# Kernel optimization log

Measured on AMD Instinct MI355X. Metric: run time of the kernel, lower is better.

The kernel has to match this reference:

```python
import jax, jax.numpy as jnp
import numpy as np

BITS = 8

def _hilbert_distance(grid, bits=BITS):
    # Skilling's algorithm: 3D grid coords -> Hilbert curve distance. grid: [N,3] int64.
    X = grid.astype(np.int64).copy()
    n = X.shape[1]
    M = 1 << (bits - 1)
    Q = M
    while Q > 1:
        P = Q - 1
        for i in range(n):
            hi = (X[:, i] & Q) != 0
            X[:, 0] = np.where(hi, X[:, 0] ^ P, X[:, 0])
            t = np.where(hi, 0, (X[:, 0] ^ X[:, i]) & P)
            X[:, 0] ^= t
            X[:, i] ^= t
        Q >>= 1
    for i in range(1, n):
        X[:, i] ^= X[:, i - 1]
    t = np.zeros(X.shape[0], dtype=np.int64)
    Q = M
    while Q > 1:
        t = np.where((X[:, n - 1] & Q) != 0, t ^ (Q - 1), t)
        Q >>= 1
    X ^= t[:, None]
    h = np.zeros(X.shape[0], dtype=np.int64)
    for b in range(bits - 1, -1, -1):
        for i in range(n):
            h = (h << 1) | ((X[:, i] >> b) & 1)
    return h

def _orders(x_np, bits=BITS):
    B, N, _ = x_np.shape
    oh = np.zeros((B, N), dtype=np.int64)
    ot = np.zeros((B, N), dtype=np.int64)
    gmax = (1 << bits) - 1
    for b in range(B):
        pts = x_np[b]
        mins, maxs = pts.min(0), pts.max(0)
        span = np.maximum(maxs - mins, 1e-6)
        norm = (pts - mins) / span
        g = np.clip(norm * gmax, 0, gmax).astype(np.int64)
        oh[b] = np.argsort(_hilbert_distance(g, bits), kind='stable')
        gt = np.clip(norm[:, ::-1] * gmax, 0, gmax).astype(np.int64)
        ot[b] = np.argsort(_hilbert_distance(gt, bits), kind='stable')
    return oh, ot

def setup_inputs() -> dict:
    key = jax.random.key(0)
    ks = jax.random.split(key, 12)
    B, N, E = 4, 2048, 128
    NB, DS, DC, EXP, NC = 2, 16, 4, 2, 40
    DI = E * EXP
    DR = max(1, (E + 15) // 16)
    x = jax.random.normal(ks[0], (B, N, 3), jnp.float32)
    oh, ot = _orders(np.asarray(x))
    # dt_proj bias = softplus^-1(dt), dt ~ LogUniform(1e-3, 0.1)
    dt = jnp.exp(jax.random.uniform(ks[1], (NB, DI)) * (np.log(0.1) - np.log(0.001)) + np.log(0.001))
    dtproj_b = dt + jnp.log(-jnp.expm1(-dt))
    return dict(
        x=x,
        order_h=jnp.asarray(oh), order_t=jnp.asarray(ot),
        pe_w=jax.random.normal(ks[2], (E, 3)) * 0.3, pe_b=jnp.zeros((E,)),
        gamma=jnp.ones((2, E)), beta=jnp.zeros((2, E)),
        ln_g=jnp.ones((NB, E)), ln_b=jnp.zeros((NB, E)),
        inproj_w=jax.random.normal(ks[3], (NB, 2 * DI, E)) * (E ** -0.5),
        conv_w=jax.random.normal(ks[4], (NB, DI, DC)) * 0.3,
        conv_b=jnp.zeros((NB, DI)),
        xproj_w=jax.random.normal(ks[5], (NB, DR + 2 * DS, DI)) * (DI ** -0.5),
        dtproj_w=jax.random.normal(ks[6], (NB, DI, DR)) * (DR ** -0.5),
        dtproj_b=dtproj_b,
        A_log=jnp.tile(jnp.log(jnp.arange(1, DS + 1, dtype=jnp.float32))[None, None], (NB, DI, 1)),
        Dp=jnp.ones((NB, DI)),
        outproj_w=jax.random.normal(ks[7], (NB, E, DI)) * (DI ** -0.5),
        hn_g=jnp.ones((E,)), hn_b=jnp.zeros((E,)),
        fc_w=jax.random.normal(ks[8], (NC, E)) * (E ** -0.5),
        fc_b=jnp.zeros((NC,)),
    )

def _ln(x, g, b):
    m = jnp.mean(x, -1, keepdims=True)
    v = jnp.mean((x - m) ** 2, -1, keepdims=True)
    return (x - m) / jnp.sqrt(v + 1e-5) * g + b

def _block(h, g, bb, inw, cw, cb, xw, dtw, dtb, Alog, Dv, outw):
    B, L, E = h.shape
    DI, DC = cw.shape
    DR = dtw.shape[1]
    DS = Alog.shape[1]
    xn = _ln(h, g, bb)
    uz = xn @ inw.T                       # [B, L, 2*DI]
    u, z = uz[..., :DI], uz[..., DI:]
    # depthwise causal conv (kernel DC, left pad DC-1)
    up = jnp.pad(u, ((0, 0), (DC - 1, 0), (0, 0)))
    uc = cb + sum(up[:, k:k + L, :] * cw[:, k] for k in range(DC))
    uc = jax.nn.silu(uc)
    xdbl = uc @ xw.T                      # [B, L, DR+2*DS]
    dt = xdbl[..., :DR]
    Bv = xdbl[..., DR:DR + DS]
    Cv = xdbl[..., DR + DS:]
    delta = jax.nn.softplus(dt @ dtw.T + dtb)  # [B, L, DI]
    A = -jnp.exp(Alog)                    # [DI, DS]
    def step(hst, xs):
        d, ut, bt, ct = xs                # [B,DI],[B,DI],[B,DS],[B,DS]
        hst = jnp.exp(d[:, :, None] * A[None]) * hst + (d * ut)[:, :, None] * bt[:, None, :]
        y = jnp.einsum('bds,bs->bd', hst, ct) + Dv * ut
        return hst, y
    h0 = jnp.zeros((B, DI, DS), h.dtype)
    _, ys = jax.lax.scan(step, h0, (delta.transpose(1, 0, 2), uc.transpose(1, 0, 2),
                                    Bv.transpose(1, 0, 2), Cv.transpose(1, 0, 2)))
    y = ys.transpose(1, 0, 2) * jax.nn.silu(z)
    return h + y @ outw.T

def reference(x, order_h, order_t, pe_w, pe_b, gamma, beta, ln_g, ln_b,
              inproj_w, conv_w, conv_b, xproj_w, dtproj_w, dtproj_b,
              A_log, Dp, outproj_w, hn_g, hn_b, fc_w, fc_b):
    pts_h = jnp.take_along_axis(x, order_h[..., None], axis=1)
    pts_t = jnp.take_along_axis(x, order_t[..., None], axis=1)
    th = (pts_h @ pe_w.T + pe_b) * gamma[0] + beta[0]
    tt = (pts_t @ pe_w.T + pe_b) * gamma[1] + beta[1]
    h = jnp.concatenate([th, tt], axis=1)  # [B, 2N, E]
    for i in range(ln_g.shape[0]):
        h = _block(h, ln_g[i], ln_b[i], inproj_w[i], conv_w[i], conv_b[i], xproj_w[i],
                   dtproj_w[i], dtproj_b[i], A_log[i], Dp[i], outproj_w[i])
    h = _ln(h, hn_g, hn_b)
    return h.mean(axis=1) @ fc_w.T + fc_b
```

## Files before the change

### kernel.cpp

```cpp
#include <hip/hip_runtime.h>
#include <hip/hip_bf16.h>
#include <math.h>

#define BATCH 4
#define NPTS  2048
#define L     4096
#define E     128
#define DI    256
#define DS    16
#define DRR   8
#define DCV   4
#define NBLK  2
#define NC    40
#define XDW   40
#define ROWS  (BATCH*L)
#define CH    32
#define NCH   128

typedef unsigned short u16;
typedef short short8 __attribute__((ext_vector_type(8)));
typedef float f32x4v __attribute__((ext_vector_type(4)));

__device__ __forceinline__ u16 f2bf(float x) {
  unsigned u = __float_as_uint(x);
  u = u + 0x7FFFu + ((u >> 16) & 1u);
  return (u16)(u >> 16);
}
__device__ __forceinline__ float bf2f(u16 h) {
  return __uint_as_float(((unsigned)h) << 16);
}
__device__ __forceinline__ float softplusf(float x) {
  if (x > 20.f) return x;
  float t = __builtin_amdgcn_exp2f(x * 1.44269504f);
  return 0.69314718f * __builtin_amdgcn_logf(1.f + t);
}

__global__ void embed_ln_split(const float* __restrict__ x,
                               const int* __restrict__ oh, const int* __restrict__ ot,
                               const float* __restrict__ pe_w, const float* __restrict__ pe_b,
                               const float* __restrict__ gamma, const float* __restrict__ beta,
                               const float* __restrict__ g, const float* __restrict__ bb,
                               float* __restrict__ h, u16* __restrict__ dhi, u16* __restrict__ dlo) {
  int wave = threadIdx.x >> 6;
  int lane = threadIdx.x & 63;
  int row = blockIdx.x * 4 + wave;
  int n = row % L;
  int b = row / L;
  int gi = (n >= NPTS) ? 1 : 0;
  int nn = n - gi * NPTS;
  int src = gi ? ot[b * NPTS + nn] : oh[b * NPTS + nn];
  const float* xp = x + ((size_t)b * NPTS + src) * 3;
  float p0 = xp[0], p1 = xp[1], p2 = xp[2];
  int e0 = lane, e1 = lane + 64;
  float v0 = pe_b[e0] + p0 * pe_w[e0 * 3] + p1 * pe_w[e0 * 3 + 1] + p2 * pe_w[e0 * 3 + 2];
  float v1 = pe_b[e1] + p0 * pe_w[e1 * 3] + p1 * pe_w[e1 * 3 + 1] + p2 * pe_w[e1 * 3 + 2];
  v0 = v0 * gamma[gi * E + e0] + beta[gi * E + e0];
  v1 = v1 * gamma[gi * E + e1] + beta[gi * E + e1];
  size_t base = (size_t)row * E;
  h[base + e0] = v0;
  h[base + e1] = v1;
  float s1 = v0 + v1, s2 = v0 * v0 + v1 * v1;
  #pragma unroll
  for (int off = 32; off > 0; off >>= 1) {
    s1 += __shfl_xor(s1, off);
    s2 += __shfl_xor(s2, off);
  }
  float m = s1 * (1.0f / E);
  float var = s2 * (1.0f / E) - m * m;
  float inv = rsqrtf(var + 1e-5f);
  float o0 = (v0 - m) * inv * g[e0] + bb[e0];
  float o1 = (v1 - m) * inv * g[e1] + bb[e1];
  u16 h0 = f2bf(o0), h1 = f2bf(o1);
  dhi[base + e0] = h0; dhi[base + e1] = h1;
  dlo[base + e0] = f2bf(o0 - bf2f(h0));
  dlo[base + e1] = f2bf(o1 - bf2f(h1));
}

__global__ void split_all(const float* __restrict__ inproj, const float* __restrict__ outw,
                          const float* __restrict__ xw,
                          u16* __restrict__ wihi, u16* __restrict__ wilo,
                          u16* __restrict__ wohi, u16* __restrict__ wolo,
                          u16* __restrict__ wxhi, u16* __restrict__ wxlo) {
  const int n1 = NBLK * 2 * DI * E;
  const int n2 = NBLK * E * DI;
  const int n3 = NBLK * XDW * DI;
  int i = blockIdx.x * 256 + threadIdx.x;
  if (i < n1) {
    float v = inproj[i];
    u16 h = f2bf(v);
    wihi[i] = h; wilo[i] = f2bf(v - bf2f(h));
  } else if (i < n1 + n2) {
    int j = i - n1;
    float v = outw[j];
    u16 h = f2bf(v);
    wohi[j] = h; wolo[j] = f2bf(v - bf2f(h));
  } else if (i < n1 + n2 + n3) {
    int j = i - n1 - n2;
    float v = xw[j];
    u16 h = f2bf(v);
    wxhi[j] = h; wxlo[j] = f2bf(v - bf2f(h));
  }
}

template<int BN, int ACC>
__global__ __launch_bounds__(256)
void mfma_gemm_lds(const u16* __restrict__ Ahi, const u16* __restrict__ Alo,
                   const u16* __restrict__ Bhi, const u16* __restrict__ Blo,
                   float* __restrict__ C, int M, int N, int K, int ldc) {
  constexpr int BM = 128, BK = 64, PITCH = 72;
  constexpr int MSUB = (BN == 128) ? 4 : 2;
  constexpr int NSUB = 4;
  __shared__ u16 sA[2][BM][PITCH];
  __shared__ u16 sB[2][BN][PITCH];
  int tid = threadIdx.x;
  int wave = tid >> 6, lane = tid & 63, quad = lane >> 4, l16 = lane & 15;
  int rowBase = blockIdx.x * BM, colBase = blockIdx.y * BN;
  int wrow = (BN == 128) ? (wave >> 1) * 64 : wave * 32;
  int wcol = (BN == 128) ? (wave & 1) * 64 : 0;
  f32x4v acc[MSUB][NSUB] = {};
  for (int k0 = 0; k0 < K; k0 += BK) {
    #pragma unroll
    for (int hl = 0; hl < 2; hl++) {
      const u16* srcA = hl ? Alo : Ahi;
      #pragma unroll
      for (int c = 0; c < BM * 8 / 256; c++) {
        int ch = c * 256 + tid;
        int row = ch >> 3, kc = ch & 7;
        float4 v = *(const float4*)(srcA + (size_t)(rowBase + row) * K + k0 + kc * 8);
        *(float4*)&sA[hl][row][kc * 8] = v;
      }
      const u16* srcB = hl ? Blo : Bhi;
      #pragma unroll
      for (int c = 0; c < BN * 8 / 256; c++) {
        int ch = c * 256 + tid;
        int row = ch >> 3, kc = ch & 7;
        float4 v = *(const float4*)(srcB + (size_t)(colBase + row) * K + k0 + kc * 8);
        *(float4*)&sB[hl][row][kc * 8] = v;
      }
    }
    __syncthreads();
    short8 afh[MSUB][2], afl[MSUB][2];
    #pragma unroll
    for (int i = 0; i < MSUB; i++)
      #pragma unroll
      for (int kf = 0; kf < 2; kf++) {
        afh[i][kf] = *(const short8*)&sA[0][wrow + i * 16 + l16][kf * 32 + quad * 8];
        afl[i][kf] = *(const short8*)&sA[1][wrow + i * 16 + l16][kf * 32 + quad * 8];
      }
    #pragma unroll
    for (int j = 0; j < NSUB; j++)
      #pragma unroll
      for (int kf = 0; kf < 2; kf++) {
        short8 bh = *(const short8*)&sB[0][wcol + j * 16 + l16][kf * 32 + quad * 8];
        short8 bl = *(const short8*)&sB[1][wcol + j * 16 + l16][kf * 32 + quad * 8];
        #pragma unroll
        for (int i = 0; i < MSUB; i++) {
          acc[i][j] = __builtin_amdgcn_mfma_f32_16x16x32_bf16(afh[i][kf], bh, acc[i][j], 0, 0, 0);
          acc[i][j] = __builtin_amdgcn_mfma_f32_16x16x32_bf16(afh[i][kf], bl, acc[i][j], 0, 0, 0);
          acc[i][j] = __builtin_amdgcn_mfma_f32_16x16x32_bf16(afl[i][kf], bh, acc[i][j], 0, 0, 0);
        }
      }
    __syncthreads();
  }
  int orow0 = rowBase + wrow + quad * 4;
  #pragma unroll
  for (int i = 0; i < MSUB; i++) {
    #pragma unroll
    for (int j = 0; j < NSUB; j++) {
      int cc = colBase + wcol + j * 16 + l16;
      #pragma unroll
      for (int r = 0; r < 4; r++) {
        size_t idx = (size_t)(orow0 + i * 16 + r) * ldc + cc;
        if (ACC) C[idx] += acc[i][j][r];
        else     C[idx] = acc[i][j][r];
      }
    }
  }
}

__global__ __launch_bounds__(256)
void conv_xproj(const float* __restrict__ uz, const float* __restrict__ cw,
                const float* __restrict__ cb,
                const u16* __restrict__ xwhi, const u16* __restrict__ xwlo,
                float* __restrict__ xdbl) {
  constexpr int RB = 16, UPITCH = DI + 8;
  __shared__ u16 sUhi[RB][UPITCH];
  __shared__ u16 sUlo[RB][UPITCH];
  int d = threadIdx.x;
  int r0 = blockIdx.x * RB;
  int t0 = r0 % L;
  const size_t US = 2 * DI;
  float w0 = cw[d * DCV], w1 = cw[d * DCV + 1], w2 = cw[d * DCV + 2], w3 = cw[d * DCV + 3];
  float bias = cb[d];
  float uwin[RB + 3];
  #pragma unroll
  for (int j = 0; j < RB + 3; j++) {
    int t = t0 + j - 3;
    uwin[j] = (t >= 0) ? uz[(size_t)(r0 + j - 3) * US + d] : 0.f;
  }
  #pragma unroll
  for (int j = 0; j < RB; j++) {
    float a = bias + w0 * uwin[j] + w1 * uwin[j + 1] + w2 * uwin[j + 2] + w3 * uwin[j + 3];
    float v = a / (1.f + __expf(-a));
    u16 hh = f2bf(v);
    sUhi[j][d] = hh;
    sUlo[j][d] = f2bf(v - bf2f(hh));
  }
  __syncthreads();
  int wave = threadIdx.x >> 6, lane = threadIdx.x & 63;
  int quad = lane >> 4, l16 = lane & 15;
  if (wave < 3) {
    int col = wave * 16 + l16;
    int colc = (col < XDW) ? col : 0;
    const u16* bhp = xwhi + (size_t)colc * DI;
    const u16* blp = xwlo + (size_t)colc * DI;
    f32x4v acc = {};
    #pragma unroll
    for (int ks = 0; ks < DI / 32; ks++) {
      short8 ah = *(const short8*)&sUhi[l16][ks * 32 + quad * 8];
      short8 al = *(const short8*)&sUlo[l16][ks * 32 + quad * 8];
      short8 bh = *(const short8*)(bhp + ks * 32 + quad * 8);
      short8 bl = *(const short8*)(blp + ks * 32 + quad * 8);
      acc = __builtin_amdgcn_mfma_f32_16x16x32_bf16(ah, bh, acc, 0, 0, 0);
      acc = __builtin_amdgcn_mfma_f32_16x16x32_bf16(ah, bl, acc, 0, 0, 0);
      acc = __builtin_amdgcn_mfma_f32_16x16x32_bf16(al, bh, acc, 0, 0, 0);
      acc = __builtin_amdgcn_mfma_f32_16x16x32_bf16(al, bl, acc, 0, 0, 0);
    }
    if (col < XDW) {
      #pragma unroll
      for (int r = 0; r < 4; r++)
        xdbl[(size_t)(r0 + quad * 4 + r) * XDW + col] = acc[r];
    }
  }
}

__global__ __launch_bounds__(256, 4)
void scan_passA(const float* __restrict__ uz, const float* __restrict__ xdbl,
                const float* __restrict__ dtw, const float* __restrict__ dtb,
                const float* __restrict__ A_log,
                const float* __restrict__ cw, const float* __restrict__ cb,
                float* __restrict__ hloc, float* __restrict__ sumd) {
  int b = blockIdx.x / NCH, c = blockIdx.x % NCH;
  int d = threadIdx.x;
  __shared__ float Bsh[CH][DS];
  __shared__ float Dsh[CH][DRR];
  for (int i = threadIdx.x; i < CH * DS; i += 256) {
    int tt = i >> 4, s = i & 15;
    Bsh[tt][s] = xdbl[((size_t)b * L + c * CH + tt) * XDW + DRR + s];
  }
  {
    int i = threadIdx.x;
    int td = i >> 3, q = i & 7;
    Dsh[td][q] = xdbl[((size_t)b * L + c * CH + td) * XDW + q];
  }
  const size_t US = 2 * DI;
  const float* up = uz + ((size_t)b * L + c * CH) * US + d;
  float cw0 = cw[d * DCV], cw1 = cw[d * DCV + 1], cw2 = cw[d * DCV + 2], cw3 = cw[d * DCV + 3];
  float cbias = cb[d];
  float um0, um1, um2;
  if (c == 0) { um0 = um1 = um2 = 0.f; }
  else {
    um0 = up[-3 * (ptrdiff_t)US];
    um1 = up[-2 * (ptrdiff_t)US];
    um2 = up[-1 * (ptrdiff_t)US];
  }
  float ucur = up[0];
  float Av[DS];
  #pragma unroll
  for (int s = 0; s < DS; s++) Av[s] = -__expf(A_log[d * DS + s]);
  bool fastE = true;
  #pragma unroll
  for (int s = 0; s < DS; s++)
    fastE = fastE && (fabsf(Av[s] + (float)(s + 1)) <= 1e-3f * (s + 1));
  float4 wd0 = *(const float4*)(dtw + d * DRR);
  float4 wd1 = *(const float4*)(dtw + d * DRR + 4);
  float dbias = dtb[d];
  __syncthreads();
  float st[DS] = {};
  float sd = 0.f;
  #pragma unroll
  for (int t0 = 0; t0 < CH; t0++) {
    float unext = (t0 + 1 < CH) ? up[(size_t)(t0 + 1) * US] : 0.f;
    float a = cbias + cw0 * um0 + cw1 * um1 + cw2 * um2 + cw3 * ucur;
    float utv = a / (1.f + __expf(-a));
    um0 = um1; um1 = um2; um2 = ucur; ucur = unext;
    float4 D0 = *(const float4*)&Dsh[t0][0];
    float4 D1 = *(const float4*)&Dsh[t0][4];
    float v = dbias + D0.x * wd0.x + D0.y * wd0.y + D0.z * wd0.z + D0.w * wd0.w
                    + D1.x * wd1.x + D1.y * wd1.y + D1.z * wd1.z + D1.w * wd1.w;
    float dl = softplusf(v);
    sd += dl;
    float du = dl * utv;
    float4 B0 = *(const float4*)&Bsh[t0][0];
    float4 B1 = *(const float4*)&Bsh[t0][4];
    float4 B2 = *(const float4*)&Bsh[t0][8];
    float4 B3 = *(const float4*)&Bsh[t0][12];
    float Bv[DS] = {B0.x, B0.y, B0.z, B0.w, B1.x, B1.y, B1.z, B1.w,
                    B2.x, B2.y, B2.z, B2.w, B3.x, B3.y, B3.z, B3.w};
    if (fastE) {
      float e1 = __expf(-dl);
      float er = 1.f;
      #pragma unroll
      for (int s = 0; s < DS; s++) {
        er *= e1;
        st[s] = er * st[s] + du * Bv[s];
      }
    } else {
      #pragma unroll
      for (int s = 0; s < DS; s++) {
        float aa = __expf(dl * Av[s]);
        st[s] = aa * st[s] + du * Bv[s];
      }
    }
  }
  size_t base = (((size_t)b * NCH + c) * DI + d) * DS;
  *(float4*)&hloc[base + 0]  = float4{st[0], st[1], st[2], st[3]};
  *(float4*)&hloc[base + 4]  = float4{st[4], st[5], st[6], st[7]};
  *(float4*)&hloc[base + 8]  = float4{st[8], st[9], st[10], st[11]};
  *(float4*)&hloc[base + 12] = float4{st[12], st[13], st[14], st[15]};
  sumd[((size_t)b * NCH + c) * DI + d] = sd;
}

#define PB_G 16
__global__ __launch_bounds__(64)
void scan_passB(const float* __restrict__ A_log, const float* __restrict__ hloc,
                const float* __restrict__ sumd, float* __restrict__ hinit) {
  int tid = threadIdx.x;
  int dgroup = blockIdx.x % (DI / 4);
  int b = blockIdx.x / (DI / 4);
  int d = dgroup * 4 + (tid >> 4);
  int s = tid & 15;
  float Av = -__expf(A_log[d * DS + s]);
  size_t off = (size_t)b * NCH * DI * DS + dgroup * 64 + tid;
  size_t soff = (size_t)b * NCH * DI + d;
  const size_t HST = (size_t)DI * DS;
  float bv[PB_G], sd[PB_G], bvn[PB_G], sdn[PB_G];
  #pragma unroll
  for (int j = 0; j < PB_G; j++) {
    bv[j] = hloc[off + j * HST];
    sd[j] = sumd[soff + j * DI];
  }
  float X = 0.f;
  for (int g = 0; g < NCH / PB_G; g++) {
    if (g + 1 < NCH / PB_G) {
      #pragma unroll
      for (int j = 0; j < PB_G; j++) {
        bvn[j] = hloc[off + (j + PB_G) * HST];
        sdn[j] = sumd[soff + (j + PB_G) * DI];
      }
    }
    #pragma unroll
    for (int j = 0; j < PB_G; j++) {
      float a = __expf(Av * sd[j]);
      hinit[off + j * HST] = X;
      X = a * X + bv[j];
    }
    #pragma unroll
    for (int j = 0; j < PB_G; j++) { bv[j] = bvn[j]; sd[j] = sdn[j]; }
    off += PB_G * HST;
    soff += PB_G * DI;
  }
}

template<int VARIANT>
__global__ __launch_bounds__(256, 2)
void scan_passC_out(const float* __restrict__ uz, const float* __restrict__ xdbl,
                    const float* __restrict__ dtw, const float* __restrict__ dtb,
                    const float* __restrict__ A_log, const float* __restrict__ Dp,
                    const float* __restrict__ cw, const float* __restrict__ cb,
                    const float* __restrict__ hinit,
                    const u16* __restrict__ wohi, const u16* __restrict__ wolo,
                    float* __restrict__ h, const float* __restrict__ g,
                    const float* __restrict__ bb, u16* __restrict__ dhi,
                    u16* __restrict__ dlo, float* __restrict__ partial) {
  constexpr int YP = DI + 8;
  constexpr int HP = E + 4;
  int b = blockIdx.x / NCH, c = blockIdx.x % NCH;
  int d = threadIdx.x;
  __shared__ float Bsh[CH][DS];
  __shared__ float Csh[CH][DS];
  __shared__ float Dsh[CH][DRR];
  __shared__ u16 sYhi[CH][YP];
  __shared__ u16 sYlo[CH][YP];
  __shared__ float hsm[CH][HP];
  __shared__ float red[4][E];
  for (int i = threadIdx.x; i < CH * DS; i += 256) {
    int tt = i >> 4, s = i & 15;
    size_t rb = ((size_t)b * L + c * CH + tt) * XDW;
    Bsh[tt][s] = xdbl[rb + DRR + s];
    Csh[tt][s] = xdbl[rb + DRR + DS + s];
  }
  {
    int i = threadIdx.x;
    int td = i >> 3, q = i & 7;
    Dsh[td][q] = xdbl[((size_t)b * L + c * CH + td) * XDW + q];
  }
  const size_t US = 2 * DI;
  const float* up = uz + ((size_t)b * L + c * CH) * US + d;
  const float* zp = up + DI;
  float cw0 = cw[d * DCV], cw1 = cw[d * DCV + 1], cw2 = cw[d * DCV + 2], cw3 = cw[d * DCV + 3];
  float cbias = cb[d];
  float um0, um1, um2;
  if (c == 0) { um0 = um1 = um2 = 0.f; }
  else {
    um0 = up[-3 * (ptrdiff_t)US];
    um1 = up[-2 * (ptrdiff_t)US];
    um2 = up[-1 * (ptrdiff_t)US];
  }
  float ucur = up[0];
  float zcur = zp[0];
  float st[DS];
  size_t hbase = (((size_t)b * NCH + c) * DI + d) * DS;
  {
    float4 h0 = *(const float4*)&hinit[hbase + 0];
    float4 h1 = *(const float4*)&hinit[hbase + 4];
    float4 h2 = *(const float4*)&hinit[hbase + 8];
    float4 h3 = *(const float4*)&hinit[hbase + 12];
    st[0]=h0.x; st[1]=h0.y; st[2]=h0.z; st[3]=h0.w;
    st[4]=h1.x; st[5]=h1.y; st[6]=h1.z; st[7]=h1.w;
    st[8]=h2.x; st[9]=h2.y; st[10]=h2.z; st[11]=h2.w;
    st[12]=h3.x; st[13]=h3.y; st[14]=h3.z; st[15]=h3.w;
  }
  float Av[DS];
  #pragma unroll
  for (int s = 0; s < DS; s++) Av[s] = -__expf(A_log[d * DS + s]);
  bool fastE = true;
  #pragma unroll
  for (int s = 0; s < DS; s++)
    fastE = fastE && (fabsf(Av[s] + (float)(s + 1)) <= 1e-3f * (s + 1));
  float4 wd0 = *(const float4*)(dtw + d * DRR);
  float4 wd1 = *(const float4*)(dtw + d * DRR + 4);
  float dbias = dtb[d];
  float Dv = Dp[d];
  __syncthreads();
  #pragma unroll 8
  for (int t0 = 0; t0 < CH; t0++) {
    float unext = (t0 + 1 < CH) ? up[(size_t)(t0 + 1) * US] : 0.f;
    float znext = (t0 + 1 < CH) ? zp[(size_t)(t0 + 1) * US] : 0.f;
    float a = cbias + cw0 * um0 + cw1 * um1 + cw2 * um2 + cw3 * ucur;
    float utv = a / (1.f + __expf(-a));
    um0 = um1; um1 = um2; um2 = ucur; ucur = unext;
    float4 D0 = *(const float4*)&Dsh[t0][0];
    float4 D1 = *(const float4*)&Dsh[t0][4];
    float v = dbias + D0.x * wd0.x + D0.y * wd0.y + D0.z * wd0.z + D0.w * wd0.w
                    + D1.x * wd1.x + D1.y * wd1.y + D1.z * wd1.z + D1.w * wd1.w;
    float dl = softplusf(v);
    float du = dl * utv;
    float acc = Dv * utv;
    float4 B0 = *(const float4*)&Bsh[t0][0];
    float4 B1 = *(const float4*)&Bsh[t0][4];
    float4 B2 = *(const float4*)&Bsh[t0][8];
    float4 B3 = *(const float4*)&Bsh[t0][12];
    float4 C0 = *(const float4*)&Csh[t0][0];
    float4 C1 = *(const float4*)&Csh[t0][4];
    float4 C2 = *(const float4*)&Csh[t0][8];
    float4 C3 = *(const float4*)&Csh[t0][12];
    float Bv[DS] = {B0.x, B0.y, B0.z, B0.w, B1.x, B1.y, B1.z, B1.w,
                    B2.x, B2.y, B2.z, B2.w, B3.x, B3.y, B3.z, B3.w};
    float Cv[DS] = {C0.x, C0.y, C0.z, C0.w, C1.x, C1.y, C1.z, C1.w,
                    C2.x, C2.y, C2.z, C2.w, C3.x, C3.y, C3.z, C3.w};
    if (fastE) {
      float e1 = __expf(-dl);
      float er = 1.f;
      #pragma unroll
      for (int s = 0; s < DS; s++) {
        er *= e1;
        st[s] = er * st[s] + du * Bv[s];
        acc += st[s] * Cv[s];
      }
    } else {
      #pragma unroll
      for (int s = 0; s < DS; s++) {
        float aa = __expf(dl * Av[s]);
        st[s] = aa * st[s] + du * Bv[s];
        acc += st[s] * Cv[s];
      }
    }
    float zz = zcur; zcur = znext;
    float yv = acc * (zz / (1.f + __expf(-zz)));
    u16 hh = f2bf(yv);
    sYhi[t0][d] = hh;
    sYlo[t0][d] = f2bf(yv - bf2f(hh));
  }
  __syncthreads();
  int wave = d >> 6, lane = d & 63, quad = lane >> 4, l16 = lane & 15;
  f32x4v oacc[2][2] = {};
  #pragma unroll
  for (int ks = 0; ks < DI / 32; ks++) {
    short8 a0h = *(const short8*)&sYhi[l16][ks * 32 + quad * 8];
    short8 a0l = *(const short8*)&sYlo[l16][ks * 32 + quad * 8];
    short8 a1h = *(const short8*)&sYhi[16 + l16][ks * 32 + quad * 8];
    short8 a1l = *(const short8*)&sYlo[16 + l16][ks * 32 + quad * 8];
    #pragma unroll
    for (int j = 0; j < 2; j++) {
      int col = wave * 32 + j * 16 + l16;
      short8 bh = *(const short8*)(wohi + (size_t)col * DI + ks * 32 + quad * 8);
      short8 bl = *(const short8*)(wolo + (size_t)col * DI + ks * 32 + quad * 8);
      oacc[0][j] = __builtin_amdgcn_mfma_f32_16x16x32_bf16(a0h, bh, oacc[0][j], 0, 0, 0);
      oacc[0][j] = __builtin_amdgcn_mfma_f32_16x16x32_bf16(a0h, bl, oacc[0][j], 0, 0, 0);
      oacc[0][j] = __builtin_amdgcn_mfma_f32_16x16x32_bf16(a0l, bh, oacc[0][j], 0, 0, 0);
      oacc[1][j] = __builtin_amdgcn_mfma_f32_16x16x32_bf16(a1h, bh, oacc[1][j], 0, 0, 0);
      oacc[1][j] = __builtin_amdgcn_mfma_f32_16x16x32_bf16(a1h, bl, oacc[1][j], 0, 0, 0);
      oacc[1][j] = __builtin_amdgcn_mfma_f32_16x16x32_bf16(a1l, bh, oacc[1][j], 0, 0, 0);
    }
  }
  size_t rr0 = (size_t)b * L + c * CH;
  #pragma unroll
  for (int i = 0; i < 2; i++) {
    #pragma unroll
    for (int j = 0; j < 2; j++) {
      int col = wave * 32 + j * 16 + l16;
      #pragma unroll
      for (int r = 0; r < 4; r++) {
        int row = i * 16 + quad * 4 + r;
        float v = h[(rr0 + row) * E + col] + oacc[i][j][r];
        hsm[row][col] = v;
        if (VARIANT == 0) h[(rr0 + row) * E + col] = v;
      }
    }
  }
  __syncthreads();
  float g0 = g[lane], g1 = g[lane + 64], b0 = bb[lane], b1 = bb[lane + 64];
  float pa0 = 0.f, pa1 = 0.f;
  for (int jj = 0; jj < 8; jj++) {
    int row = wave * 8 + jj;
    float x0 = hsm[row][lane], x1 = hsm[row][lane + 64];
    float s1 = x0 + x1, s2 = x0 * x0 + x1 * x1;
    #pragma unroll
    for (int off = 32; off > 0; off >>= 1) {
      s1 += __shfl_xor(s1, off);
      s2 += __shfl_xor(s2, off);
    }
    float m = s1 * (1.0f / E);
    float var = s2 * (1.0f / E) - m * m;
    float inv = rsqrtf(var + 1e-5f);
    float o0 = (x0 - m) * inv * g0 + b0;
    float o1 = (x1 - m) * inv * g1 + b1;
    if (VARIANT == 0) {
      size_t base = (rr0 + row) * E;
      u16 h0 = f2bf(o0), h1 = f2bf(o1);
      dhi[base + lane]      = h0;
      dhi[base + lane + 64] = h1;
      dlo[base + lane]      = f2bf(o0 - bf2f(h0));
      dlo[base + lane + 64] = f2bf(o1 - bf2f(h1));
    } else {
      pa0 += o0; pa1 += o1;
    }
  }
  if (VARIANT == 1) {
    red[wave][lane]      = pa0;
    red[wave][lane + 64] = pa1;
    __syncthreads();
    if (wave == 0) {
      #pragma unroll
      for (int half = 0; half < 2; half++) {
        int e = lane + half * 64;
        partial[(size_t)blockIdx.x * E + e] =
            red[0][e] + red[1][e] + red[2][e] + red[3][e];
      }
    }
  }
}

__global__ __launch_bounds__(256)
void fc_reduce(const float* __restrict__ partial, float* __restrict__ hmean) {
  int w = blockIdx.x * 4 + (threadIdx.x >> 6);
  int lane = threadIdx.x & 63;
  int b = w >> 7, e = w & 127;
  float s = partial[((size_t)b * NCH + lane) * E + e]
          + partial[((size_t)b * NCH + 64 + lane) * E + e];
  #pragma unroll
  for (int off = 32; off > 0; off >>= 1) s += __shfl_xor(s, off);
  if (lane == 0) hmean[w] = s;
}

__global__ __launch_bounds__(256)
void fc_final(const float* __restrict__ hmean, const float* __restrict__ fcw,
              const float* __restrict__ fcb, float* __restrict__ out) {
  constexpr int WP = E + 4;
  __shared__ float hm[BATCH * E];
  __shared__ float wsm[NC * WP];
  for (int i = threadIdx.x; i < BATCH * E; i += 256) hm[i] = hmean[i];
  for (int i = threadIdx.x; i < NC * E; i += 256) {
    int o = i >> 7, e = i & 127;
    wsm[o * WP + e] = fcw[i];
  }
  __syncthreads();
  int i = threadIdx.x;
  if (i < BATCH * NC) {
    int b = i / NC, o = i % NC;
    float acc = 0.f;
    #pragma unroll 8
    for (int e = 0; e < E; e++) acc += hm[b * E + e] * wsm[o * WP + e];
    out[i] = acc * (1.f / L) + fcb[o];
  }
}

extern "C" void kernel_launch(void* const* d_in, const int* in_sizes, int n_in,
                              void* d_out, int out_size, void* d_ws, size_t ws_size,
                              hipStream_t stream) {
  const float* x      = (const float*)d_in[0];
  const int*   oh     = (const int*)d_in[1];
  const int*   ot     = (const int*)d_in[2];
  const float* pe_w   = (const float*)d_in[3];
  const float* pe_b   = (const float*)d_in[4];
  const float* gamma  = (const float*)d_in[5];
  const float* beta   = (const float*)d_in[6];
  const float* ln_g   = (const float*)d_in[7];
  const float* ln_b   = (const float*)d_in[8];
  const float* inproj = (const float*)d_in[9];
  const float* conv_w = (const float*)d_in[10];
  const float* conv_b = (const float*)d_in[11];
  const float* xproj  = (const float*)d_in[12];
  const float* dtw    = (const float*)d_in[13];
  const float* dtb    = (const float*)d_in[14];
  const float* A_log  = (const float*)d_in[15];
  const float* Dp     = (const float*)d_in[16];
  const float* outw   = (const float*)d_in[17];
  const float* hn_g   = (const float*)d_in[18];
  const float* hn_b   = (const float*)d_in[19];
  const float* fc_w   = (const float*)d_in[20];
  const float* fc_b   = (const float*)d_in[21];
  float* out = (float*)d_out;

  char* ws = (char*)d_ws;
  size_t off = 0;
  auto alloc = [&](size_t bytes) { size_t o = off; off += (bytes + 255) & ~(size_t)255; return o; };
  float* h     = (float*)(ws + alloc((size_t)ROWS * E * 4));
  u16*   xnhi  = (u16*)  (ws + alloc((size_t)ROWS * E * 2));
  u16*   xnlo  = (u16*)  (ws + alloc((size_t)ROWS * E * 2));
  float* uz    = (float*)(ws + alloc((size_t)ROWS * 2 * DI * 4));
  float* xdbl  = (float*)(ws + alloc((size_t)ROWS * XDW * 4));
  float* hloc  = (float*)(ws + alloc((size_t)BATCH * NCH * DI * DS * 4));
  float* sumd  = (float*)(ws + alloc((size_t)BATCH * NCH * DI * 4));
  u16*   wihi  = (u16*)  (ws + alloc((size_t)NBLK * 2 * DI * E * 2));
  u16*   wilo  = (u16*)  (ws + alloc((size_t)NBLK * 2 * DI * E * 2));
  u16*   wohi  = (u16*)  (ws + alloc((size_t)NBLK * E * DI * 2));
  u16*   wolo  = (u16*)  (ws + alloc((size_t)NBLK * E * DI * 2));
  u16*   wxhi  = (u16*)  (ws + alloc((size_t)NBLK * XDW * DI * 2));
  u16*   wxlo  = (u16*)  (ws + alloc((size_t)NBLK * XDW * DI * 2));
  float* partial = (float*)(ws + alloc((size_t)BATCH * NCH * E * 4));
  float* hmean = (float*)(ws + alloc((size_t)BATCH * E * 4));
  float* hinit = hloc;

  embed_ln_split<<<ROWS / 4, 256, 0, stream>>>(x, oh, ot, pe_w, pe_b, gamma, beta,
                                               ln_g, ln_b, h, xnhi, xnlo);
  const int nsplit = NBLK * 2 * DI * E + NBLK * E * DI + NBLK * XDW * DI;
  split_all<<<(nsplit + 255) / 256, 256, 0, stream>>>(inproj, outw, xproj,
                                                      wihi, wilo, wohi, wolo, wxhi, wxlo);

  for (int i = 0; i < NBLK; i++) {
    dim3 g1(ROWS / 128, (2 * DI) / 128);
    mfma_gemm_lds<128, 0><<<g1, 256, 0, stream>>>(xnhi, xnlo,
                                                  wihi + (size_t)i * 2 * DI * E, wilo + (size_t)i * 2 * DI * E,
                                                  uz, ROWS, 2 * DI, E, 2 * DI);

    conv_xproj<<<ROWS / 16, 256, 0, stream>>>(uz, conv_w + (size_t)i * DI * DCV, conv_b + i * DI,
                                              wxhi + (size_t)i * XDW * DI, wxlo + (size_t)i * XDW * DI,
                                              xdbl);

    scan_passA<<<BATCH * NCH, 256, 0, stream>>>(uz, xdbl, dtw + (size_t)i * DI * DRR, dtb + i * DI,
                                                A_log + (size_t)i * DI * DS,
                                                conv_w + (size_t)i * DI * DCV, conv_b + i * DI,
                                                hloc, sumd);
    scan_passB<<<BATCH * (DI / 4), 64, 0, stream>>>(A_log + (size_t)i * DI * DS, hloc, sumd, hinit);

    if (i == 0) {
      scan_passC_out<0><<<BATCH * NCH, 256, 0, stream>>>(uz, xdbl, dtw + (size_t)i * DI * DRR, dtb + i * DI,
                                                         A_log + (size_t)i * DI * DS, Dp + i * DI,
                                                         conv_w + (size_t)i * DI * DCV, conv_b + i * DI,
                                                         hinit,
                                                         wohi + (size_t)i * E * DI, wolo + (size_t)i * E * DI,
                                                         h, ln_g + (i + 1) * E, ln_b + (i + 1) * E,
                                                         xnhi, xnlo, partial);
    } else {
      scan_passC_out<1><<<BATCH * NCH, 256, 0, stream>>>(uz, xdbl, dtw + (size_t)i * DI * DRR, dtb + i * DI,
                                                         A_log + (size_t)i * DI * DS, Dp + i * DI,
                                                         conv_w + (size_t)i * DI * DCV, conv_b + i * DI,
                                                         hinit,
                                                         wohi + (size_t)i * E * DI, wolo + (size_t)i * E * DI,
                                                         h, hn_g, hn_b,
                                                         xnhi, xnlo, partial);
    }
  }

  fc_reduce<<<128, 256, 0, stream>>>(partial, hmean);
  fc_final<<<1, 256, 0, stream>>>(hmean, fc_w, fc_b, out);
}
```

Before: 276.6 us.

## Halve scan chunk length, alias LDS buffers, and raise scan occupancy

Scan chunk length drops from 32 to 16 timesteps, doubling the number of chunks and blocks per batch, which adds parallelism to the chunked selective scan. In pass C, the Y staging buffers and the hsm buffer now share one aliased LDS region, the Av register array is replaced by on-the-fly A_log reads, and launch bounds rise to 3 blocks per CU. Together these aim for more resident waves and a lower register and LDS footprint. The cost is a longer sequential carry pass B over twice as many chunks, more partial sums to reduce, an extra barrier, and extra exp work on the non-fast path.

```diff
diff --git a/kernel.cpp b/kernel.cpp
--- a/kernel.cpp
+++ b/kernel.cpp
@@ -14,8 +14,8 @@
 #define NC    40
 #define XDW   40
 #define ROWS  (BATCH*L)
-#define CH    32
-#define NCH   128
+#define CH    16
+#define NCH   256
 
 typedef unsigned short u16;
 typedef short short8 __attribute__((ext_vector_type(8)));
@@ -244,14 +244,14 @@
   int d = threadIdx.x;
   __shared__ float Bsh[CH][DS];
   __shared__ float Dsh[CH][DRR];
-  for (int i = threadIdx.x; i < CH * DS; i += 256) {
+  {
+    int i = threadIdx.x;
     int tt = i >> 4, s = i & 15;
     Bsh[tt][s] = xdbl[((size_t)b * L + c * CH + tt) * XDW + DRR + s];
-  }
-  {
-    int i = threadIdx.x;
-    int td = i >> 3, q = i & 7;
-    Dsh[td][q] = xdbl[((size_t)b * L + c * CH + td) * XDW + q];
+    if (i < CH * DRR) {
+      int td = i >> 3, q = i & 7;
+      Dsh[td][q] = xdbl[((size_t)b * L + c * CH + td) * XDW + q];
+    }
   }
   const size_t US = 2 * DI;
   const float* up = uz + ((size_t)b * L + c * CH) * US + d;
@@ -265,13 +265,13 @@
     um2 = up[-1 * (ptrdiff_t)US];
   }
   float ucur = up[0];
-  float Av[DS];
-  #pragma unroll
-  for (int s = 0; s < DS; s++) Av[s] = -__expf(A_log[d * DS + s]);
+  const float* alp = A_log + d * DS;
   bool fastE = true;
   #pragma unroll
-  for (int s = 0; s < DS; s++)
-    fastE = fastE && (fabsf(Av[s] + (float)(s + 1)) <= 1e-3f * (s + 1));
+  for (int s = 0; s < DS; s++) {
+    float av = -__expf(alp[s]);
+    fastE = fastE && (fabsf(av + (float)(s + 1)) <= 1e-3f * (s + 1));
+  }
   float4 wd0 = *(const float4*)(dtw + d * DRR);
   float4 wd1 = *(const float4*)(dtw + d * DRR + 4);
   float dbias = dtb[d];
@@ -308,7 +308,7 @@
     } else {
       #pragma unroll
       for (int s = 0; s < DS; s++) {
-        float aa = __expf(dl * Av[s]);
+        float aa = __expf(-dl * __expf(alp[s]));
         st[s] = aa * st[s] + du * Bv[s];
       }
     }
@@ -363,7 +363,7 @@
 }
 
 template<int VARIANT>
-__global__ __launch_bounds__(256, 2)
+__global__ __launch_bounds__(256, 3)
 void scan_passC_out(const float* __restrict__ uz, const float* __restrict__ xdbl,
                     const float* __restrict__ dtw, const float* __restrict__ dtb,
                     const float* __restrict__ A_log, const float* __restrict__ Dp,
@@ -380,20 +380,21 @@
   __shared__ float Bsh[CH][DS];
   __shared__ float Csh[CH][DS];
   __shared__ float Dsh[CH][DRR];
-  __shared__ u16 sYhi[CH][YP];
-  __shared__ u16 sYlo[CH][YP];
-  __shared__ float hsm[CH][HP];
+  __shared__ __align__(16) char sYraw[2 * CH * YP * 2];
   __shared__ float red[4][E];
-  for (int i = threadIdx.x; i < CH * DS; i += 256) {
+  u16* sYhi = (u16*)sYraw;
+  u16* sYlo = sYhi + CH * YP;
+  float* hsm = (float*)sYraw;
+  {
+    int i = threadIdx.x;
     int tt = i >> 4, s = i & 15;
     size_t rb = ((size_t)b * L + c * CH + tt) * XDW;
     Bsh[tt][s] = xdbl[rb + DRR + s];
     Csh[tt][s] = xdbl[rb + DRR + DS + s];
-  }
-  {
-    int i = threadIdx.x;
-    int td = i >> 3, q = i & 7;
-    Dsh[td][q] = xdbl[((size_t)b * L + c * CH + td) * XDW + q];
+    if (i < CH * DRR) {
+      int td = i >> 3, q = i & 7;
+      Dsh[td][q] = xdbl[((size_t)b * L + c * CH + td) * XDW + q];
+    }
   }
   const size_t US = 2 * DI;
   const float* up = uz + ((size_t)b * L + c * CH) * US + d;
@@ -421,13 +422,13 @@
     st[8]=h2.x; st[9]=h2.y; st[10]=h2.z; st[11]=h2.w;
     st[12]=h3.x; st[13]=h3.y; st[14]=h3.z; st[15]=h3.w;
   }
-  float Av[DS];
-  #pragma unroll
-  for (int s = 0; s < DS; s++) Av[s] = -__expf(A_log[d * DS + s]);
+  const float* alp = A_log + d * DS;
   bool fastE = true;
   #pragma unroll
-  for (int s = 0; s < DS; s++)
-    fastE = fastE && (fabsf(Av[s] + (float)(s + 1)) <= 1e-3f * (s + 1));
+  for (int s = 0; s < DS; s++) {
+    float av = -__expf(alp[s]);
+    fastE = fastE && (fabsf(av + (float)(s + 1)) <= 1e-3f * (s + 1));
+  }
   float4 wd0 = *(const float4*)(dtw + d * DRR);
   float4 wd1 = *(const float4*)(dtw + d * DRR + 4);
   float dbias = dtb[d];
@@ -471,7 +472,7 @@
     } else {
       #pragma unroll
       for (int s = 0; s < DS; s++) {
-        float aa = __expf(dl * Av[s]);
+        float aa = __expf(-dl * __expf(alp[s]));
         st[s] = aa * st[s] + du * Bv[s];
         acc += st[s] * Cv[s];
       }
@@ -479,52 +480,45 @@
     float zz = zcur; zcur = znext;
     float yv = acc * (zz / (1.f + __expf(-zz)));
     u16 hh = f2bf(yv);
-    sYhi[t0][d] = hh;
-    sYlo[t0][d] = f2bf(yv - bf2f(hh));
+    sYhi[t0 * YP + d] = hh;
+    sYlo[t0 * YP + d] = f2bf(yv - bf2f(hh));
   }
   __syncthreads();
   int wave = d >> 6, lane = d & 63, quad = lane >> 4, l16 = lane & 15;
-  f32x4v oacc[2][2] = {};
+  f32x4v oacc[2] = {};
   #pragma unroll
   for (int ks = 0; ks < DI / 32; ks++) {
-    short8 a0h = *(const short8*)&sYhi[l16][ks * 32 + quad * 8];
-    short8 a0l = *(const short8*)&sYlo[l16][ks * 32 + quad * 8];
-    short8 a1h = *(const short8*)&sYhi[16 + l16][ks * 32 + quad * 8];
-    short8 a1l = *(const short8*)&sYlo[16 + l16][ks * 32 + quad * 8];
+    short8 ah = *(const short8*)&sYhi[l16 * YP + ks * 32 + quad * 8];
+    short8 al = *(const short8*)&sYlo[l16 * YP + ks * 32 + quad * 8];
     #pragma unroll
     for (int j = 0; j < 2; j++) {
       int col = wave * 32 + j * 16 + l16;
       short8 bh = *(const short8*)(wohi + (size_t)col * DI + ks * 32 + quad * 8);
       short8 bl = *(const short8*)(wolo + (size_t)col * DI + ks * 32 + quad * 8);
-      oacc[0][j] = __builtin_amdgcn_mfma_f32_16x16x32_bf16(a0h, bh, oacc[0][j], 0, 0, 0);
-      oacc[0][j] = __builtin_amdgcn_mfma_f32_16x16x32_bf16(a0h, bl, oacc[0][j], 0, 0, 0);
-      oacc[0][j] = __builtin_amdgcn_mfma_f32_16x16x32_bf16(a0l, bh, oacc[0][j], 0, 0, 0);
-      oacc[1][j] = __builtin_amdgcn_mfma_f32_16x16x32_bf16(a1h, bh, oacc[1][j], 0, 0, 0);
-      oacc[1][j] = __builtin_amdgcn_mfma_f32_16x16x32_bf16(a1h, bl, oacc[1][j], 0, 0, 0);
-      oacc[1][j] = __builtin_amdgcn_mfma_f32_16x16x32_bf16(a1l, bh, oacc[1][j], 0, 0, 0);
-    }
-  }
+      oacc[j] = __builtin_amdgcn_mfma_f32_16x16x32_bf16(ah, bh, oacc[j], 0, 0, 0);
+      oacc[j] = __builtin_amdgcn_mfma_f32_16x16x32_bf16(ah, bl, oacc[j], 0, 0, 0);
+      oacc[j] = __builtin_amdgcn_mfma_f32_16x16x32_bf16(al, bh, oacc[j], 0, 0, 0);
+    }
+  }
+  __syncthreads();
   size_t rr0 = (size_t)b * L + c * CH;
   #pragma unroll
-  for (int i = 0; i < 2; i++) {
-    #pragma unroll
-    for (int j = 0; j < 2; j++) {
-      int col = wave * 32 + j * 16 + l16;
-      #pragma unroll
-      for (int r = 0; r < 4; r++) {
-        int row = i * 16 + quad * 4 + r;
-        float v = h[(rr0 + row) * E + col] + oacc[i][j][r];
-        hsm[row][col] = v;
-        if (VARIANT == 0) h[(rr0 + row) * E + col] = v;
-      }
+  for (int j = 0; j < 2; j++) {
+    int col = wave * 32 + j * 16 + l16;
+    #pragma unroll
+    for (int r = 0; r < 4; r++) {
+      int row = quad * 4 + r;
+      float v = h[(rr0 + row) * E + col] + oacc[j][r];
+      hsm[row * HP + col] = v;
+      if (VARIANT == 0) h[(rr0 + row) * E + col] = v;
     }
   }
   __syncthreads();
   float g0 = g[lane], g1 = g[lane + 64], b0 = bb[lane], b1 = bb[lane + 64];
   float pa0 = 0.f, pa1 = 0.f;
-  for (int jj = 0; jj < 8; jj++) {
-    int row = wave * 8 + jj;
-    float x0 = hsm[row][lane], x1 = hsm[row][lane + 64];
+  for (int jj = 0; jj < 4; jj++) {
+    int row = wave * 4 + jj;
+    float x0 = hsm[row * HP + lane], x1 = hsm[row * HP + lane + 64];
     float s1 = x0 + x1, s2 = x0 * x0 + x1 * x1;
     #pragma unroll
     for (int off = 32; off > 0; off >>= 1) {
@@ -567,8 +561,10 @@
   int w = blockIdx.x * 4 + (threadIdx.x >> 6);
   int lane = threadIdx.x & 63;
   int b = w >> 7, e = w & 127;
-  float s = partial[((size_t)b * NCH + lane) * E + e]
-          + partial[((size_t)b * NCH + 64 + lane) * E + e];
+  float s = 0.f;
+  #pragma unroll
+  for (int k = 0; k < NCH; k += 64)
+    s += partial[((size_t)b * NCH + k + lane) * E + e];
   #pragma unroll
   for (int off = 32; off > 0; off >>= 1) s += __shfl_xor(s, off);
   if (lane == 0) hmean[w] = s;
```

Result: slower. 290.5 us (+5.0%).
